# Optimization experiments

Hardware: AMD Instinct MI355X
Metric: run time of the kernel (lower is better)

Reference implementation:

```python
import jax, jax.numpy as jnp
import numpy as np

NUM_RULES = 256
IN_F = 2048
OUT_F = 2048
RANK = 8
BLOCK = 64
NUM_BLOCKS = min(IN_F, OUT_F) // BLOCK  # 32
SHARED_RANK = int(round(np.sqrt(min(IN_F, OUT_F))))  # 45
N = 16384


def setup_inputs() -> dict:
    key = jax.random.key(0)
    ks = jax.random.split(key, 7)
    x = jax.random.normal(ks[0], (N, IN_F), dtype=jnp.float32)
    rule_ids = jax.random.randint(ks[1], (N,), 0, NUM_RULES, dtype=jnp.int32)
    shared_in = jax.random.normal(ks[2], (IN_F, SHARED_RANK), dtype=jnp.float32) * (1.0 / np.sqrt(IN_F))
    shared_out = jax.random.normal(ks[3], (SHARED_RANK, OUT_F), dtype=jnp.float32) * (1.0 / np.sqrt(SHARED_RANK))
    rule_in = jax.random.normal(ks[4], (NUM_RULES, BLOCK, RANK), dtype=jnp.float32) * (1.0 / np.sqrt(BLOCK))
    rule_out = jax.random.normal(ks[5], (NUM_RULES, RANK, BLOCK), dtype=jnp.float32) * (1.0 / np.sqrt(RANK))
    rule_block_logits = jax.random.normal(ks[6], (NUM_RULES, NUM_BLOCKS), dtype=jnp.float32) * (1.0 / np.sqrt(NUM_BLOCKS))
    return {"x": x, "rule_ids": rule_ids, "shared_in": shared_in, "shared_out": shared_out,
            "rule_in": rule_in, "rule_out": rule_out, "rule_block_logits": rule_block_logits}


def reference(x, rule_ids, shared_in, shared_out, rule_in, rule_out, rule_block_logits):
    # Shared low-rank path: [N, in] @ [in, r] @ [r, out]
    base_out = (x @ shared_in) @ shared_out  # [N, OUT_F]

    total = NUM_BLOCKS * BLOCK
    x_blocks = x[:, :total].reshape(-1, NUM_BLOCKS, BLOCK)  # [N, B, bs]

    # Per-token gather of rule adapter params. This is mathematically
    # identical to the torch sort/pad/bmm/scatter path (zero padding
    # contributes zero), expressed as a dense gather + batched einsum.
    r_in = rule_in[rule_ids]    # [N, bs, RANK]
    r_out = rule_out[rule_ids]  # [N, RANK, bs]
    hidden = jnp.einsum('nbs,nsr->nbr', x_blocks, r_in)     # [N, B, RANK]
    adapter = jnp.einsum('nbr,nrs->nbs', hidden, r_out)     # [N, B, bs]

    # Block selector softmax with temperature 1/sqrt(num_blocks)
    inv_temp = jnp.sqrt(jnp.float32(NUM_BLOCKS))
    sel = jax.nn.softmax(rule_block_logits[rule_ids] * inv_temp, axis=-1)  # [N, B]
    weighted = (adapter * sel[:, :, None]).reshape(-1, total)  # [N, total]

    adapter_full = jnp.zeros_like(base_out).at[:, :total].set(weighted.astype(base_out.dtype))
    return base_out + adapter_full
```

## Files before the change

### kernel.cpp

```cpp
#include <hip/hip_runtime.h>
#include <hip/hip_bf16.h>
#include <math.h>

#define NTOK  16384
#define INF   2048
#define OUTF  2048
#define SR    45
#define RANK  8
#define BLK   64
#define NBLK  32
#define NRULE 256
#define NHIST 32
#define MAXSLOT (NTOK + NRULE * 15)
#define NTILE16 (MAXSLOT / 16)

typedef __attribute__((ext_vector_type(8))) short bf16x8;
typedef __attribute__((ext_vector_type(4))) float f32x4;
typedef __attribute__((ext_vector_type(4))) short s16x4;

typedef const __attribute__((address_space(1))) unsigned int GU32;
typedef __attribute__((address_space(3))) unsigned int LU32;

#define MFMA __builtin_amdgcn_mfma_f32_16x16x32_bf16
#define SBAR() __builtin_amdgcn_sched_barrier(0)

__device__ inline short f2bs(float f) {
    __hip_bfloat16 h = __float2bfloat16(f);
    return *reinterpret_cast<short*>(&h);
}
__device__ inline bf16x8 cvt8(const float4& a, const float4& b) {
    bf16x8 r;
    r[0] = f2bs(a.x); r[1] = f2bs(a.y); r[2] = f2bs(a.z); r[3] = f2bs(a.w);
    r[4] = f2bs(b.x); r[5] = f2bs(b.y); r[6] = f2bs(b.z); r[7] = f2bs(b.w);
    return r;
}

__global__ void kprep_a(const int* __restrict__ rule_ids,
                        const float* __restrict__ shared_in,
                        const float* __restrict__ shared_out,
                        const float* __restrict__ rule_in,
                        const float* __restrict__ rule_out,
                        unsigned short* __restrict__ ssb,
                        unsigned short* __restrict__ sob,
                        unsigned short* __restrict__ rinf,
                        unsigned short* __restrict__ rof,
                        int* __restrict__ ghist_part,
                        int* __restrict__ perm_p,
                        int* __restrict__ srid_p)
{
    if (blockIdx.x < 128) {
        const int tid = blockIdx.x * 256 + threadIdx.x;
        const int stride = 128 * 256;
        for (int idx = tid; idx < 64 * 3 * 512; idx += stride) {
            int ch = idx / 1536, rem = idx - ch * 1536;
            int nf = rem / 512;
            int l = (rem >> 3) & 63, j = idx & 7;
            int k = ch * 32 + ((l >> 4) << 3) + j;
            int col = nf * 16 + (l & 15);
            ssb[idx] = (col < SR) ? (unsigned short)f2bs(shared_in[(size_t)k * SR + col]) : 0;
        }
        for (int idx = tid; idx < 128 * 2 * 512; idx += stride) {
            int CF = idx >> 10;
            int kc = (idx >> 9) & 1;
            int l = (idx >> 3) & 63, j = idx & 7;
            int k = kc * 32 + ((l >> 4) << 3) + j;
            int col = CF * 16 + (l & 15);
            sob[idx] = (k < SR) ? (unsigned short)f2bs(shared_out[(size_t)k * OUTF + col]) : 0;
        }
        for (int idx = tid; idx < NRULE * 2 * 512; idx += stride) {
            int rid = idx >> 10;
            int half = (idx >> 9) & 1;
            int l = (idx >> 3) & 63, j = idx & 7;
            int r = l & 15;
            int s = half * 32 + ((l >> 4) << 3) + j;
            rinf[idx] = (r < RANK) ? (unsigned short)f2bs(rule_in[(size_t)rid * 512 + s * RANK + r]) : 0;
        }
        for (int idx = tid; idx < NRULE * 4 * 512; idx += stride) {
            int rid = idx >> 11;
            int cf = (idx >> 9) & 3;
            int l = (idx >> 3) & 63, j = idx & 7;
            int k = ((l >> 4) << 3) + j;
            int c = cf * 16 + (l & 15);
            rof[idx] = (k < RANK) ? (unsigned short)f2bs(rule_out[(size_t)rid * 512 + k * BLK + c]) : 0;
        }
    } else {
        __shared__ int lh[NRULE];
        const int tid = threadIdx.x;
        const int hb = blockIdx.x - 128;
        lh[tid] = 0;
        __syncthreads();
        const int base = hb * 512;
        atomicAdd(&lh[rule_ids[base + tid]], 1);
        atomicAdd(&lh[rule_ids[base + 256 + tid]], 1);
        __syncthreads();
        ghist_part[hb * NRULE + tid] = lh[tid];
        for (int j = tid; j < MAXSLOT / 32; j += 256) {
            int idx = hb * (MAXSLOT / 32) + j;
            perm_p[idx] = -1;
            srid_p[idx] = 0;
        }
    }
}

__global__ void kprep_scan(const int* __restrict__ ghist_part,
                           const float* __restrict__ logits,
                           int* __restrict__ gcnt,
                           int* __restrict__ srid_p,
                           float* __restrict__ sel_t,
                           int* __restrict__ ntot)
{
    __shared__ int sc[NRULE];
    const int tid = threadIdx.x;
    int h = 0;
#pragma unroll
    for (int b = 0; b < NHIST; ++b) h += ghist_part[b * NRULE + tid];
    const int pd = (h + 15) & ~15;
    sc[tid] = pd;
    for (int off = 1; off < NRULE; off <<= 1) {
        __syncthreads();
        int v = (tid >= off) ? sc[tid - off] : 0;
        __syncthreads();
        sc[tid] += v;
    }
    __syncthreads();
    const int excl = sc[tid] - pd;
    gcnt[tid] = excl;
    for (int q = h; q < pd; ++q) srid_p[excl + q] = tid;
    if (tid == NRULE - 1) *ntot = sc[tid];
    const float invT = 5.65685424949238f;
    const float* __restrict__ lg = logits + (size_t)tid * NBLK;
    float m = -1e30f;
    for (int b = 0; b < NBLK; ++b) m = fmaxf(m, lg[b] * invT);
    float s = 0.0f;
    for (int b = 0; b < NBLK; ++b) s += expf(lg[b] * invT - m);
    const float inv = 1.0f / s;
    for (int b = 0; b < NBLK; ++b)
        sel_t[(size_t)tid * NBLK + b] = expf(lg[b] * invT - m) * inv;
}

__global__ void kprep_scatter(const int* __restrict__ rule_ids,
                              int* __restrict__ gcnt,
                              int* __restrict__ perm_p,
                              int* __restrict__ srid_p)
{
    const int i = blockIdx.x * 256 + threadIdx.x;
    const int r = rule_ids[i];
    const int p = atomicAdd(&gcnt[r], 1);
    perm_p[p] = i;
    srid_p[p] = r;
}

__global__ __launch_bounds__(128, 4)
void kmain(const float* __restrict__ x,
           const int* __restrict__ perm_p,
           const int* __restrict__ srid_p,
           const unsigned short* __restrict__ ssb,
           const unsigned short* __restrict__ sob,
           const unsigned short* __restrict__ rinf,
           const unsigned short* __restrict__ rof,
           const float* __restrict__ sel_t,
           const int* __restrict__ ntot,
           float* __restrict__ out)
{
    __shared__ __align__(16) float xbuf[2][1024];
    __shared__ __align__(16) float hstmp[2][2][16][8];
    __shared__ __align__(16) unsigned short hs_lds[16][264];
    __shared__ __align__(16) unsigned short t_bf[16][72];

#define TRD(W, SL, C) (((float*)xbuf)[((W) * 16 + (SL)) * 52 + (C)])

    const int slot0 = blockIdx.x * 16;
    if (slot0 >= *ntot) return;

    const int tid  = threadIdx.x;
    const int lane = tid & 63;
    const int kh   = tid >> 6;
    const int row_l = lane & 15, grp = lane >> 4;

    const int rid_u = __builtin_amdgcn_readfirstlane(srid_p[slot0]);

    const int r0 = tid >> 4;
    const int u  = tid & 15;
    int tokA = perm_p[slot0 + r0];      if (tokA < 0) tokA = 0;
    int tokB = perm_p[slot0 + r0 + 8];  if (tokB < 0) tokB = 0;
    const char* gA = (const char*)(x + (size_t)tokA * INF) + ((u ^ (r0 & 7)) << 4);
    const char* gB = (const char*)(x + (size_t)tokB * INF) + ((u ^ (r0 & 7)) << 4);

#define STAGE(CH) do { \
        char* _lb = (char*)xbuf + (((CH) & 1) << 12) + (kh << 10); \
        const size_t _o = (size_t)(CH) << 8; \
        __builtin_amdgcn_global_load_lds((GU32*)(gA + _o), (LU32*)_lb,          16, 0, 0); \
        __builtin_amdgcn_global_load_lds((GU32*)(gB + _o), (LU32*)(_lb + 2048), 16, 0, 0); \
    } while (0)

    const int offA = (row_l * 16 + ((kh * 8 + grp * 2 + 0) ^ (row_l & 7))) << 4;
    const int offB = (row_l * 16 + ((kh * 8 + grp * 2 + 1) ^ (row_l & 7))) << 4;

    const bf16x8 ri = *(const bf16x8*)(rinf + ((size_t)rid_u * 2 + kh) * 512 + lane * 8);

    f32x4 aT0 = {0.f, 0.f, 0.f, 0.f};
    f32x4 aT1 = {0.f, 0.f, 0.f, 0.f};
    f32x4 aT2 = {0.f, 0.f, 0.f, 0.f};

    STAGE(0);
    __syncthreads();

    for (int ch = 0; ch < 32; ++ch) {
        if (ch < 31) STAGE(ch + 1);
        if (ch > 0) {
            const int b = ch - 1, pb = b & 1;
            const int sl = tid >> 3, r = tid & 7;
            const float v = hstmp[pb][0][sl][r] + hstmp[pb][1][sl][r];
            hs_lds[sl][b * 8 + r] =
                (unsigned short)f2bs(v * sel_t[(size_t)rid_u * NBLK + b]);
        }
        {
            const char* xb = (const char*)xbuf + ((ch & 1) << 12);
            const float4 fa = *(const float4*)(xb + offA);
            const float4 fb = *(const float4*)(xb + offB);
            const bf16x8 af = cvt8(fa, fb);
            const unsigned short* sp = ssb + (size_t)(ch * 2 + kh) * 1536 + lane * 8;
            f32x4 aH = {0.f, 0.f, 0.f, 0.f};
            aT0 = MFMA(af, *(const bf16x8*)(sp),        aT0, 0, 0, 0);
            aT1 = MFMA(af, *(const bf16x8*)(sp + 512),  aT1, 0, 0, 0);
            aT2 = MFMA(af, *(const bf16x8*)(sp + 1024), aT2, 0, 0, 0);
            aH  = MFMA(af, ri, aH, 0, 0, 0);
            if (row_l < RANK) {
#pragma unroll
                for (int q = 0; q < 4; ++q)
                    hstmp[ch & 1][kh][(grp << 2) + q][row_l] = aH[q];
            }
        }
        __syncthreads();
    }

    {
        const int b = 31, pb = 1;
        const int sl = tid >> 3, r = tid & 7;
        const float v = hstmp[pb][0][sl][r] + hstmp[pb][1][sl][r];
        hs_lds[sl][b * 8 + r] =
            (unsigned short)f2bs(v * sel_t[(size_t)rid_u * NBLK + b]);
    }
#pragma unroll
    for (int q = 0; q < 4; ++q) {
        const int sl = (grp << 2) + q;
        TRD(kh, sl, row_l)      = aT0[q];
        TRD(kh, sl, 16 + row_l) = aT1[q];
        TRD(kh, sl, 32 + row_l) = aT2[q];
    }
    __syncthreads();
    {
        const int sl = tid >> 3;
        const int cidx = tid & 7;
        if (cidx < 6) {
            const int c0 = cidx << 3;
            s16x4 v0, v1;
#pragma unroll
            for (int j = 0; j < 4; ++j) {
                v0[j] = f2bs(TRD(0, sl, c0 + j)     + TRD(1, sl, c0 + j));
                v1[j] = f2bs(TRD(0, sl, c0 + 4 + j) + TRD(1, sl, c0 + 4 + j));
            }
            *(s16x4*)(&t_bf[sl][c0])     = v0;
            *(s16x4*)(&t_bf[sl][c0 + 4]) = v1;
        } else {
            const int c0 = 48 + ((cidx - 6) << 3);
            const s16x4 z = {0, 0, 0, 0};
            *(s16x4*)(&t_bf[sl][c0])     = z;
            *(s16x4*)(&t_bf[sl][c0 + 4]) = z;
        }
    }
    __syncthreads();

    {
        const int p = kh;
        const bf16x8 at0 = *(const bf16x8*)(&t_bf[row_l][grp << 3]);
        const bf16x8 at1 = *(const bf16x8*)(&t_bf[row_l][32 + (grp << 3)]);

        bf16x8 rfv[4];
#pragma unroll
        for (int i = 0; i < 4; ++i)
            rfv[i] = *(const bf16x8*)(rof + ((size_t)rid_u * 4 + i) * 512 + lane * 8);

        const int4 pv = *(const int4*)(perm_p + slot0 + (grp << 2));
        float* const orow0 = out + (size_t)(pv.x < 0 ? 0 : pv.x) * OUTF;
        float* const orow1 = out + (size_t)(pv.y < 0 ? 0 : pv.y) * OUTF;
        float* const orow2 = out + (size_t)(pv.z < 0 ? 0 : pv.z) * OUTF;
        float* const orow3 = out + (size_t)(pv.w < 0 ? 0 : pv.w) * OUTF;

        const int CF0 = p * 64;
        const int bb0 = p * 16;
        const unsigned short* __restrict__ sobw = sob + (size_t)CF0 * 1024 + lane * 8;

        bf16x8 sb[4][2];
        bf16x8 ah[2];
        const bf16x8 zz = {0, 0, 0, 0, 0, 0, 0, 0};

#define LOADQ(SL, QI) do { \
        const unsigned short* _sp = sobw + (size_t)(QI) * 1024; \
        sb[SL][0] = *(const bf16x8*)(_sp); \
        sb[SL][1] = *(const bf16x8*)(_sp + 512); \
    } while (0)
#define LOADA(SL, BI) do { \
        ah[SL] = zz; \
        if (lane < 16) \
            ah[SL] = *(const bf16x8*)(&hs_lds[lane][(bb0 + (BI)) * 8]); \
    } while (0)

        LOADQ(0, 0); LOADQ(1, 1); LOADQ(2, 2);
        LOADA(0, 0);
        SBAR();

#pragma unroll
        for (int qi = 0; qi < 64; ++qi) {
            if (qi < 61) LOADQ((qi + 3) & 3, qi + 3);
            if ((qi & 3) == 0 && qi < 60) LOADA(((qi >> 2) + 1) & 1, (qi >> 2) + 1);
            SBAR();
            f32x4 acc = {0.f, 0.f, 0.f, 0.f};
            acc = MFMA(at0, sb[qi & 3][0], acc, 0, 0, 0);
            acc = MFMA(at1, sb[qi & 3][1], acc, 0, 0, 0);
            acc = MFMA(ah[(qi >> 2) & 1], rfv[qi & 3], acc, 0, 0, 0);
            const int col = ((CF0 + qi) << 4) + row_l;
            if (pv.x >= 0) orow0[col] = acc[0];
            if (pv.y >= 0) orow1[col] = acc[1];
            if (pv.z >= 0) orow2[col] = acc[2];
            if (pv.w >= 0) orow3[col] = acc[3];
            SBAR();
        }
#undef LOADQ
#undef LOADA
    }
}

extern "C" void kernel_launch(void* const* d_in, const int* in_sizes, int n_in,
                              void* d_out, int out_size, void* d_ws, size_t ws_size,
                              hipStream_t stream)
{
    const float* x          = (const float*)d_in[0];
    const int*   rule_ids   = (const int*)  d_in[1];
    const float* shared_in  = (const float*)d_in[2];
    const float* shared_out = (const float*)d_in[3];
    const float* rule_in    = (const float*)d_in[4];
    const float* rule_out   = (const float*)d_in[5];
    const float* logits     = (const float*)d_in[6];
    float* out = (float*)d_out;

    char* p = (char*)d_ws;
    auto carve = [&p](size_t bytes) {
        char* r = p;
        p += (bytes + 255) & ~(size_t)255;
        return r;
    };
    int*            perm_p = (int*)carve(MAXSLOT * 4);
    int*            srid_p = (int*)carve(MAXSLOT * 4);
    unsigned short* ssb    = (unsigned short*)carve(64 * 3 * 512 * 2);
    unsigned short* sob    = (unsigned short*)carve(128 * 2 * 512 * 2);
    unsigned short* rinf   = (unsigned short*)carve((size_t)NRULE * 2 * 512 * 2);
    unsigned short* rof    = (unsigned short*)carve((size_t)NRULE * 4 * 512 * 2);
    float*          sel_t  = (float*)carve((size_t)NRULE * NBLK * 4);
    int*            ghistp = (int*)carve((size_t)NHIST * NRULE * 4);
    int*            gcnt   = (int*)carve(NRULE * 4);
    int*            ntot   = (int*)carve(4);

    kprep_a<<<dim3(160), dim3(256), 0, stream>>>(
        rule_ids, shared_in, shared_out, rule_in, rule_out,
        ssb, sob, rinf, rof, ghistp, perm_p, srid_p);
    kprep_scan<<<dim3(1), dim3(256), 0, stream>>>(
        ghistp, logits, gcnt, srid_p, sel_t, ntot);
    kprep_scatter<<<dim3(64), dim3(256), 0, stream>>>(
        rule_ids, gcnt, perm_p, srid_p);
    kmain<<<dim3(NTILE16), dim3(128), 0, stream>>>(
        x, perm_p, srid_p, ssb, sob, rinf, rof, sel_t, ntot, out);
}
```

Before: 88.80 us.

## Triple-buffer x staging and register-prefetch shared weights with explicit vmcnt waits

Staging of x chunks into LDS moves from double to triple buffering with a prefetch distance of two. The shared-weight fragments become register-prefetched two chunks ahead through inline global_load_dwordx4, tracked with manual s_waitcnt vmcnt counts in place of a plain __syncthreads per iteration. The per-rule selector weights are cached in LDS once instead of being reread from global memory every chunk. The goal is to hide global-load latency in the main K loop, at the cost of more LDS and VGPRs and fragile hand-counted waitcnt logic.

```diff
diff --git a/kernel.cpp b/kernel.cpp
--- a/kernel.cpp
+++ b/kernel.cpp
@@ -23,6 +23,15 @@
 
 #define MFMA __builtin_amdgcn_mfma_f32_16x16x32_bf16
 #define SBAR() __builtin_amdgcn_sched_barrier(0)
+
+#define VMCNT(n) do { asm volatile("s_waitcnt vmcnt(" #n ")" ::: "memory"); \
+                      __builtin_amdgcn_sched_barrier(0); } while (0)
+#define BARL()   do { __builtin_amdgcn_sched_barrier(0); \
+                      asm volatile("s_waitcnt lgkmcnt(0)" ::: "memory"); \
+                      __builtin_amdgcn_s_barrier(); \
+                      __builtin_amdgcn_sched_barrier(0); } while (0)
+#define GLOAD(dst, ptr) \
+    asm volatile("global_load_dwordx4 %0, %1, off" : "=v"(dst) : "v"(ptr) : "memory")
 
 __device__ inline short f2bs(float f) {
     __hip_bfloat16 h = __float2bfloat16(f);
@@ -162,10 +171,11 @@
            const int* __restrict__ ntot,
            float* __restrict__ out)
 {
-    __shared__ __align__(16) float xbuf[2][1024];
+    __shared__ __align__(16) float xbuf[3][1024];
     __shared__ __align__(16) float hstmp[2][2][16][8];
     __shared__ __align__(16) unsigned short hs_lds[16][264];
     __shared__ __align__(16) unsigned short t_bf[16][72];
+    __shared__ float sel_lds[NBLK];
 
 #define TRD(W, SL, C) (((float*)xbuf)[((W) * 16 + (SL)) * 52 + (C)])
 
@@ -187,43 +197,55 @@
     const char* gB = (const char*)(x + (size_t)tokB * INF) + ((u ^ (r0 & 7)) << 4);
 
 #define STAGE(CH) do { \
-        char* _lb = (char*)xbuf + (((CH) & 1) << 12) + (kh << 10); \
+        char* _lb = (char*)xbuf + (size_t)((CH) % 3) * 4096 + (kh << 10); \
         const size_t _o = (size_t)(CH) << 8; \
         __builtin_amdgcn_global_load_lds((GU32*)(gA + _o), (LU32*)_lb,          16, 0, 0); \
         __builtin_amdgcn_global_load_lds((GU32*)(gB + _o), (LU32*)(_lb + 2048), 16, 0, 0); \
     } while (0)
 
+#define WLOAD(SLOT, CH) do { \
+        const unsigned short* _wp = ssb + (size_t)((CH) * 2 + kh) * 1536 + lane * 8; \
+        GLOAD(wreg[SLOT][0], _wp); \
+        GLOAD(wreg[SLOT][1], _wp + 512); \
+        GLOAD(wreg[SLOT][2], _wp + 1024); \
+    } while (0)
+
     const int offA = (row_l * 16 + ((kh * 8 + grp * 2 + 0) ^ (row_l & 7))) << 4;
     const int offB = (row_l * 16 + ((kh * 8 + grp * 2 + 1) ^ (row_l & 7))) << 4;
 
     const bf16x8 ri = *(const bf16x8*)(rinf + ((size_t)rid_u * 2 + kh) * 512 + lane * 8);
+    if (tid < NBLK) sel_lds[tid] = sel_t[(size_t)rid_u * NBLK + tid];
 
     f32x4 aT0 = {0.f, 0.f, 0.f, 0.f};
     f32x4 aT1 = {0.f, 0.f, 0.f, 0.f};
     f32x4 aT2 = {0.f, 0.f, 0.f, 0.f};
-
-    STAGE(0);
-    __syncthreads();
-
+    bf16x8 wreg[2][3];
+
+    __syncthreads();
+
+    STAGE(0); WLOAD(0, 0);
+    STAGE(1); WLOAD(1, 1);
+
+#pragma unroll
     for (int ch = 0; ch < 32; ++ch) {
-        if (ch < 31) STAGE(ch + 1);
+        if (ch < 31) VMCNT(5); else VMCNT(0);
+        BARL();
+        if (ch < 30) STAGE(ch + 2);
         if (ch > 0) {
             const int b = ch - 1, pb = b & 1;
             const int sl = tid >> 3, r = tid & 7;
             const float v = hstmp[pb][0][sl][r] + hstmp[pb][1][sl][r];
-            hs_lds[sl][b * 8 + r] =
-                (unsigned short)f2bs(v * sel_t[(size_t)rid_u * NBLK + b]);
+            hs_lds[sl][b * 8 + r] = (unsigned short)f2bs(v * sel_lds[b]);
         }
         {
-            const char* xb = (const char*)xbuf + ((ch & 1) << 12);
+            const char* xb = (const char*)xbuf + (size_t)(ch % 3) * 4096;
             const float4 fa = *(const float4*)(xb + offA);
             const float4 fb = *(const float4*)(xb + offB);
             const bf16x8 af = cvt8(fa, fb);
-            const unsigned short* sp = ssb + (size_t)(ch * 2 + kh) * 1536 + lane * 8;
             f32x4 aH = {0.f, 0.f, 0.f, 0.f};
-            aT0 = MFMA(af, *(const bf16x8*)(sp),        aT0, 0, 0, 0);
-            aT1 = MFMA(af, *(const bf16x8*)(sp + 512),  aT1, 0, 0, 0);
-            aT2 = MFMA(af, *(const bf16x8*)(sp + 1024), aT2, 0, 0, 0);
+            aT0 = MFMA(af, wreg[ch & 1][0], aT0, 0, 0, 0);
+            aT1 = MFMA(af, wreg[ch & 1][1], aT1, 0, 0, 0);
+            aT2 = MFMA(af, wreg[ch & 1][2], aT2, 0, 0, 0);
             aH  = MFMA(af, ri, aH, 0, 0, 0);
             if (row_l < RANK) {
 #pragma unroll
@@ -231,15 +253,15 @@
                     hstmp[ch & 1][kh][(grp << 2) + q][row_l] = aH[q];
             }
         }
-        __syncthreads();
-    }
+        if (ch < 30) WLOAD(ch & 1, ch + 2);
+    }
+    __syncthreads();
 
     {
         const int b = 31, pb = 1;
         const int sl = tid >> 3, r = tid & 7;
         const float v = hstmp[pb][0][sl][r] + hstmp[pb][1][sl][r];
-        hs_lds[sl][b * 8 + r] =
-            (unsigned short)f2bs(v * sel_t[(size_t)rid_u * NBLK + b]);
+        hs_lds[sl][b * 8 + r] = (unsigned short)f2bs(v * sel_lds[b]);
     }
 #pragma unroll
     for (int q = 0; q < 4; ++q) {
```

Result: no change. 88.77 us (-0.0%).

## Stage whole x tile as bf16 in LDS and split K across four waves

Applied to the files above, without the earlier changes.

Replaces the double-buffered per-chunk async global-to-LDS pipeline with a single up-front load of each 16-token tile of x. It converts the tile to bf16 in registers and stores it into a 64KB swizzled LDS buffer. The block grows to four waves that split the K dimension of the shared and rule input projections, which removes the 32 per-chunk barriers and the hstmp reduction. The partial sums are then combined across four waves, and each wave writes half as many output columns. The cost is much higher LDS use per block, which limits occupancy to about two blocks per CU, and no overlap between loading x and the MFMA work.

```diff
diff --git a/kernel.cpp b/kernel.cpp
--- a/kernel.cpp
+++ b/kernel.cpp
@@ -17,9 +17,6 @@
 typedef __attribute__((ext_vector_type(8))) short bf16x8;
 typedef __attribute__((ext_vector_type(4))) float f32x4;
 typedef __attribute__((ext_vector_type(4))) short s16x4;
-
-typedef const __attribute__((address_space(1))) unsigned int GU32;
-typedef __attribute__((address_space(3))) unsigned int LU32;
 
 #define MFMA __builtin_amdgcn_mfma_f32_16x16x32_bf16
 #define SBAR() __builtin_amdgcn_sched_barrier(0)
@@ -150,7 +147,7 @@
     srid_p[p] = r;
 }
 
-__global__ __launch_bounds__(128, 4)
+__global__ __launch_bounds__(256, 2)
 void kmain(const float* __restrict__ x,
            const int* __restrict__ perm_p,
            const int* __restrict__ srid_p,
@@ -162,117 +159,101 @@
            const int* __restrict__ ntot,
            float* __restrict__ out)
 {
-    __shared__ __align__(16) float xbuf[2][1024];
-    __shared__ __align__(16) float hstmp[2][2][16][8];
+    __shared__ __align__(16) unsigned short xbf[16 * 2048];
     __shared__ __align__(16) unsigned short hs_lds[16][264];
     __shared__ __align__(16) unsigned short t_bf[16][72];
 
-#define TRD(W, SL, C) (((float*)xbuf)[((W) * 16 + (SL)) * 52 + (C)])
+#define TRD(W, SL, C) (((float*)xbf)[((W) * 16 + (SL)) * 52 + (C)])
 
     const int slot0 = blockIdx.x * 16;
     if (slot0 >= *ntot) return;
 
     const int tid  = threadIdx.x;
     const int lane = tid & 63;
-    const int kh   = tid >> 6;
+    const int w    = tid >> 6;
     const int row_l = lane & 15, grp = lane >> 4;
 
     const int rid_u = __builtin_amdgcn_readfirstlane(srid_p[slot0]);
 
-    const int r0 = tid >> 4;
-    const int u  = tid & 15;
-    int tokA = perm_p[slot0 + r0];      if (tokA < 0) tokA = 0;
-    int tokB = perm_p[slot0 + r0 + 8];  if (tokB < 0) tokB = 0;
-    const char* gA = (const char*)(x + (size_t)tokA * INF) + ((u ^ (r0 & 7)) << 4);
-    const char* gB = (const char*)(x + (size_t)tokB * INF) + ((u ^ (r0 & 7)) << 4);
-
-#define STAGE(CH) do { \
-        char* _lb = (char*)xbuf + (((CH) & 1) << 12) + (kh << 10); \
-        const size_t _o = (size_t)(CH) << 8; \
-        __builtin_amdgcn_global_load_lds((GU32*)(gA + _o), (LU32*)_lb,          16, 0, 0); \
-        __builtin_amdgcn_global_load_lds((GU32*)(gB + _o), (LU32*)(_lb + 2048), 16, 0, 0); \
-    } while (0)
-
-    const int offA = (row_l * 16 + ((kh * 8 + grp * 2 + 0) ^ (row_l & 7))) << 4;
-    const int offB = (row_l * 16 + ((kh * 8 + grp * 2 + 1) ^ (row_l & 7))) << 4;
-
-    const bf16x8 ri = *(const bf16x8*)(rinf + ((size_t)rid_u * 2 + kh) * 512 + lane * 8);
+    {
+        const int sr = tid >> 4;
+        const int su = tid & 15;
+        int stok = perm_p[slot0 + sr];  if (stok < 0) stok = 0;
+        const float* __restrict__ xrow = x + (size_t)stok * INF;
+        const int swz = sr & 7;
+        unsigned short* __restrict__ xd = xbf + sr * 2048;
+#pragma unroll
+        for (int j = 0; j < 16; ++j) {
+            const int u8 = j * 16 + su;
+            const float4 a = *(const float4*)(xrow + (u8 << 3));
+            const float4 b = *(const float4*)(xrow + (u8 << 3) + 4);
+            *(bf16x8*)(xd + ((u8 ^ swz) << 3)) = cvt8(a, b);
+        }
+    }
+
+    const bf16x8 ri0 = *(const bf16x8*)(rinf + ((size_t)rid_u * 2 + 0) * 512 + lane * 8);
+    const bf16x8 ri1 = *(const bf16x8*)(rinf + ((size_t)rid_u * 2 + 1) * 512 + lane * 8);
+
+    __syncthreads();
 
     f32x4 aT0 = {0.f, 0.f, 0.f, 0.f};
     f32x4 aT1 = {0.f, 0.f, 0.f, 0.f};
     f32x4 aT2 = {0.f, 0.f, 0.f, 0.f};
 
-    STAGE(0);
-    __syncthreads();
-
-    for (int ch = 0; ch < 32; ++ch) {
-        if (ch < 31) STAGE(ch + 1);
-        if (ch > 0) {
-            const int b = ch - 1, pb = b & 1;
-            const int sl = tid >> 3, r = tid & 7;
-            const float v = hstmp[pb][0][sl][r] + hstmp[pb][1][sl][r];
-            hs_lds[sl][b * 8 + r] =
-                (unsigned short)f2bs(v * sel_t[(size_t)rid_u * NBLK + b]);
-        }
-        {
-            const char* xb = (const char*)xbuf + ((ch & 1) << 12);
-            const float4 fa = *(const float4*)(xb + offA);
-            const float4 fb = *(const float4*)(xb + offB);
-            const bf16x8 af = cvt8(fa, fb);
-            const unsigned short* sp = ssb + (size_t)(ch * 2 + kh) * 1536 + lane * 8;
-            f32x4 aH = {0.f, 0.f, 0.f, 0.f};
+    const int xswz = row_l & 7;
+    const unsigned short* __restrict__ xrd = xbf + row_l * 2048;
+
+#pragma unroll
+    for (int ci = 0; ci < 8; ++ci) {
+        const int c = (w << 3) + ci;
+        f32x4 aH = {0.f, 0.f, 0.f, 0.f};
+#pragma unroll
+        for (int s = 0; s < 2; ++s) {
+            const int u8 = (c << 3) + (s << 2) + grp;
+            const bf16x8 af = *(const bf16x8*)(xrd + ((u8 ^ xswz) << 3));
+            const unsigned short* __restrict__ sp =
+                ssb + (size_t)(c * 2 + s) * 1536 + lane * 8;
             aT0 = MFMA(af, *(const bf16x8*)(sp),        aT0, 0, 0, 0);
             aT1 = MFMA(af, *(const bf16x8*)(sp + 512),  aT1, 0, 0, 0);
             aT2 = MFMA(af, *(const bf16x8*)(sp + 1024), aT2, 0, 0, 0);
-            aH  = MFMA(af, ri, aH, 0, 0, 0);
-            if (row_l < RANK) {
-#pragma unroll
-                for (int q = 0; q < 4; ++q)
-                    hstmp[ch & 1][kh][(grp << 2) + q][row_l] = aH[q];
-            }
-        }
-        __syncthreads();
-    }
-
-    {
-        const int b = 31, pb = 1;
-        const int sl = tid >> 3, r = tid & 7;
-        const float v = hstmp[pb][0][sl][r] + hstmp[pb][1][sl][r];
-        hs_lds[sl][b * 8 + r] =
-            (unsigned short)f2bs(v * sel_t[(size_t)rid_u * NBLK + b]);
-    }
+            aH  = MFMA(af, s ? ri1 : ri0, aH, 0, 0, 0);
+        }
+        const float sel = sel_t[(size_t)rid_u * NBLK + c];
+        if (row_l < RANK) {
+#pragma unroll
+            for (int q = 0; q < 4; ++q)
+                hs_lds[(grp << 2) + q][c * 8 + row_l] =
+                    (unsigned short)f2bs(aH[q] * sel);
+        }
+    }
+    __syncthreads();
+
 #pragma unroll
     for (int q = 0; q < 4; ++q) {
         const int sl = (grp << 2) + q;
-        TRD(kh, sl, row_l)      = aT0[q];
-        TRD(kh, sl, 16 + row_l) = aT1[q];
-        TRD(kh, sl, 32 + row_l) = aT2[q];
+        TRD(w, sl, row_l)      = aT0[q];
+        TRD(w, sl, 16 + row_l) = aT1[q];
+        TRD(w, sl, 32 + row_l) = aT2[q];
     }
     __syncthreads();
     {
-        const int sl = tid >> 3;
-        const int cidx = tid & 7;
-        if (cidx < 6) {
-            const int c0 = cidx << 3;
-            s16x4 v0, v1;
+        const int sl = tid >> 4;
+        const int c0 = (tid & 15) << 2;
+        s16x4 v = {0, 0, 0, 0};
+        if (c0 < 48) {
 #pragma unroll
             for (int j = 0; j < 4; ++j) {
-                v0[j] = f2bs(TRD(0, sl, c0 + j)     + TRD(1, sl, c0 + j));
-                v1[j] = f2bs(TRD(0, sl, c0 + 4 + j) + TRD(1, sl, c0 + 4 + j));
+                const float sm = TRD(0, sl, c0 + j) + TRD(1, sl, c0 + j)
+                               + TRD(2, sl, c0 + j) + TRD(3, sl, c0 + j);
+                v[j] = f2bs(sm);
             }
-            *(s16x4*)(&t_bf[sl][c0])     = v0;
-            *(s16x4*)(&t_bf[sl][c0 + 4]) = v1;
-        } else {
-            const int c0 = 48 + ((cidx - 6) << 3);
-            const s16x4 z = {0, 0, 0, 0};
-            *(s16x4*)(&t_bf[sl][c0])     = z;
-            *(s16x4*)(&t_bf[sl][c0 + 4]) = z;
-        }
+        }
+        *(s16x4*)(&t_bf[sl][c0]) = v;
     }
     __syncthreads();
 
     {
-        const int p = kh;
+        const int p = w;
         const bf16x8 at0 = *(const bf16x8*)(&t_bf[row_l][grp << 3]);
         const bf16x8 at1 = *(const bf16x8*)(&t_bf[row_l][32 + (grp << 3)]);
 
@@ -287,8 +268,8 @@
         float* const orow2 = out + (size_t)(pv.z < 0 ? 0 : pv.z) * OUTF;
         float* const orow3 = out + (size_t)(pv.w < 0 ? 0 : pv.w) * OUTF;
 
-        const int CF0 = p * 64;
-        const int bb0 = p * 16;
+        const int CF0 = p * 32;
+        const int bb0 = p * 8;
         const unsigned short* __restrict__ sobw = sob + (size_t)CF0 * 1024 + lane * 8;
 
         bf16x8 sb[4][2];
@@ -311,9 +292,9 @@
         SBAR();
 
 #pragma unroll
-        for (int qi = 0; qi < 64; ++qi) {
-            if (qi < 61) LOADQ((qi + 3) & 3, qi + 3);
-            if ((qi & 3) == 0 && qi < 60) LOADA(((qi >> 2) + 1) & 1, (qi >> 2) + 1);
+        for (int qi = 0; qi < 32; ++qi) {
+            if (qi < 29) LOADQ((qi + 3) & 3, qi + 3);
+            if ((qi & 3) == 0 && qi < 28) LOADA(((qi >> 2) + 1) & 1, (qi >> 2) + 1);
             SBAR();
             f32x4 acc = {0.f, 0.f, 0.f, 0.f};
             acc = MFMA(at0, sb[qi & 3][0], acc, 0, 0, 0);
@@ -368,6 +349,6 @@
         ghistp, logits, gcnt, srid_p, sel_t, ntot);
     kprep_scatter<<<dim3(64), dim3(256), 0, stream>>>(
         rule_ids, gcnt, perm_p, srid_p);
-    kmain<<<dim3(NTILE16), dim3(128), 0, stream>>>(
+    kmain<<<dim3(NTILE16), dim3(256), 0, stream>>>(
         x, perm_p, srid_p, ssb, sob, rinf, rof, sel_t, ntot, out);
 }
```

Result: slower. 100.3 us (+12.9%).

## Split K across waves with per-wave x pipeline and register-prefetched weights

Applied to the files above, without the earlier changes.

Each wave now owns half of the K chunks (16 blocks) with its own double-buffered x staging in LDS and inline-asm prefetch of the shared_in weights into registers, waiting on vmcnt instead of block-wide barriers each chunk. The per-block hidden partials no longer need cross-wave reduction through hstmp since each wave computes full 64-wide blocks, and selector weights are preloaded. The intent is to remove the 32 per-iteration __syncthreads and hide global latency, at the cost of more LDS and registers, so occupancy drops from 4 to 3 blocks per CU.

```diff
diff --git a/kernel.cpp b/kernel.cpp
--- a/kernel.cpp
+++ b/kernel.cpp
@@ -23,6 +23,11 @@
 
 #define MFMA __builtin_amdgcn_mfma_f32_16x16x32_bf16
 #define SBAR() __builtin_amdgcn_sched_barrier(0)
+
+#define VMCNT(n) do { asm volatile("s_waitcnt vmcnt(" #n ")" ::: "memory"); \
+                      __builtin_amdgcn_sched_barrier(0); } while (0)
+#define GLOAD(dst, ptr) \
+    asm volatile("global_load_dwordx4 %0, %1, off" : "=v"(dst) : "v"(ptr) : "memory")
 
 __device__ inline short f2bs(float f) {
     __hip_bfloat16 h = __float2bfloat16(f);
@@ -150,7 +155,7 @@
     srid_p[p] = r;
 }
 
-__global__ __launch_bounds__(128, 4)
+__global__ __launch_bounds__(128, 3)
 void kmain(const float* __restrict__ x,
            const int* __restrict__ perm_p,
            const int* __restrict__ srid_p,
@@ -162,91 +167,120 @@
            const int* __restrict__ ntot,
            float* __restrict__ out)
 {
-    __shared__ __align__(16) float xbuf[2][1024];
-    __shared__ __align__(16) float hstmp[2][2][16][8];
+    __shared__ __align__(16) char xq[2][8192];
     __shared__ __align__(16) unsigned short hs_lds[16][264];
     __shared__ __align__(16) unsigned short t_bf[16][72];
 
-#define TRD(W, SL, C) (((float*)xbuf)[((W) * 16 + (SL)) * 52 + (C)])
+#define TRD(W, SL, C) (((float*)xq)[((W) * 16 + (SL)) * 52 + (C)])
 
     const int slot0 = blockIdx.x * 16;
     if (slot0 >= *ntot) return;
 
     const int tid  = threadIdx.x;
     const int lane = tid & 63;
-    const int kh   = tid >> 6;
+    const int w    = tid >> 6;
     const int row_l = lane & 15, grp = lane >> 4;
+    const int cbase = w * 16;
 
     const int rid_u = __builtin_amdgcn_readfirstlane(srid_p[slot0]);
 
-    const int r0 = tid >> 4;
-    const int u  = tid & 15;
-    int tokA = perm_p[slot0 + r0];      if (tokA < 0) tokA = 0;
-    int tokB = perm_p[slot0 + r0 + 8];  if (tokB < 0) tokB = 0;
-    const char* gA = (const char*)(x + (size_t)tokA * INF) + ((u ^ (r0 & 7)) << 4);
-    const char* gB = (const char*)(x + (size_t)tokB * INF) + ((u ^ (r0 & 7)) << 4);
-
-#define STAGE(CH) do { \
-        char* _lb = (char*)xbuf + (((CH) & 1) << 12) + (kh << 10); \
-        const size_t _o = (size_t)(CH) << 8; \
-        __builtin_amdgcn_global_load_lds((GU32*)(gA + _o), (LU32*)_lb,          16, 0, 0); \
-        __builtin_amdgcn_global_load_lds((GU32*)(gB + _o), (LU32*)(_lb + 2048), 16, 0, 0); \
-    } while (0)
-
-    const int offA = (row_l * 16 + ((kh * 8 + grp * 2 + 0) ^ (row_l & 7))) << 4;
-    const int offB = (row_l * 16 + ((kh * 8 + grp * 2 + 1) ^ (row_l & 7))) << 4;
-
-    const bf16x8 ri = *(const bf16x8*)(rinf + ((size_t)rid_u * 2 + kh) * 512 + lane * 8);
+    const char* gsrc0; const char* gsrc1; const char* gsrc2; const char* gsrc3;
+    {
+        const int u = lane & 15;
+        const char* t[4];
+#pragma unroll
+        for (int v = 0; v < 4; ++v) {
+            const int row = 4 * v + (lane >> 4);
+            int tok = perm_p[slot0 + row];
+            if (tok < 0) tok = 0;
+            t[v] = (const char*)(x + (size_t)tok * INF) + ((u ^ (row & 7)) << 4);
+        }
+        gsrc0 = t[0]; gsrc1 = t[1]; gsrc2 = t[2]; gsrc3 = t[3];
+    }
+
+    const bf16x8 ri0 = *(const bf16x8*)(rinf + ((size_t)rid_u * 2 + 0) * 512 + lane * 8);
+    const bf16x8 ri1 = *(const bf16x8*)(rinf + ((size_t)rid_u * 2 + 1) * 512 + lane * 8);
+    float sel16[16];
+#pragma unroll
+    for (int ci = 0; ci < 16; ++ci)
+        sel16[ci] = sel_t[(size_t)rid_u * NBLK + cbase + ci];
+
+    const int swz = row_l & 7;
+    const int off00 = row_l * 256 + (((0 + grp * 2 + 0) ^ swz) << 4);
+    const int off01 = row_l * 256 + (((0 + grp * 2 + 1) ^ swz) << 4);
+    const int off10 = row_l * 256 + (((8 + grp * 2 + 0) ^ swz) << 4);
+    const int off11 = row_l * 256 + (((8 + grp * 2 + 1) ^ swz) << 4);
 
     f32x4 aT0 = {0.f, 0.f, 0.f, 0.f};
     f32x4 aT1 = {0.f, 0.f, 0.f, 0.f};
     f32x4 aT2 = {0.f, 0.f, 0.f, 0.f};
-
-    STAGE(0);
+    bf16x8 wreg[2][6];
+
+    char* const xw = xq[w];
+
+#define STAGE(SL, CI) do { \
+        char* _lb = xw + ((SL) << 12); \
+        const size_t _o = (size_t)(cbase + (CI)) << 8; \
+        __builtin_amdgcn_global_load_lds((GU32*)(gsrc0 + _o), (LU32*)_lb,          16, 0, 0); \
+        __builtin_amdgcn_global_load_lds((GU32*)(gsrc1 + _o), (LU32*)(_lb + 1024), 16, 0, 0); \
+        __builtin_amdgcn_global_load_lds((GU32*)(gsrc2 + _o), (LU32*)(_lb + 2048), 16, 0, 0); \
+        __builtin_amdgcn_global_load_lds((GU32*)(gsrc3 + _o), (LU32*)(_lb + 3072), 16, 0, 0); \
+    } while (0)
+
+#define WLOAD(SL, CI) do { \
+        const unsigned short* _w0 = ssb + (size_t)((cbase + (CI)) * 2) * 1536 + lane * 8; \
+        GLOAD(wreg[SL][0], _w0); \
+        GLOAD(wreg[SL][1], _w0 + 512); \
+        GLOAD(wreg[SL][2], _w0 + 1024); \
+        GLOAD(wreg[SL][3], _w0 + 1536); \
+        GLOAD(wreg[SL][4], _w0 + 2048); \
+        GLOAD(wreg[SL][5], _w0 + 2560); \
+    } while (0)
+
+    VMCNT(0);
+
+    STAGE(0, 0); WLOAD(0, 0);
+    STAGE(1, 1); WLOAD(1, 1);
+
+#pragma unroll
+    for (int ci = 0; ci < 16; ++ci) {
+        if (ci < 15) { VMCNT(10); } else { VMCNT(0); }
+        const int sl = ci & 1;
+        const char* xb = xw + (sl << 12);
+        f32x4 aH = {0.f, 0.f, 0.f, 0.f};
+        {
+            const float4 fa0 = *(const float4*)(xb + off00);
+            const float4 fa1 = *(const float4*)(xb + off01);
+            const bf16x8 af0 = cvt8(fa0, fa1);
+            aT0 = MFMA(af0, wreg[sl][0], aT0, 0, 0, 0);
+            aT1 = MFMA(af0, wreg[sl][1], aT1, 0, 0, 0);
+            aT2 = MFMA(af0, wreg[sl][2], aT2, 0, 0, 0);
+            aH  = MFMA(af0, ri0, aH, 0, 0, 0);
+            const float4 fb0 = *(const float4*)(xb + off10);
+            const float4 fb1 = *(const float4*)(xb + off11);
+            const bf16x8 af1 = cvt8(fb0, fb1);
+            aT0 = MFMA(af1, wreg[sl][3], aT0, 0, 0, 0);
+            aT1 = MFMA(af1, wreg[sl][4], aT1, 0, 0, 0);
+            aT2 = MFMA(af1, wreg[sl][5], aT2, 0, 0, 0);
+            aH  = MFMA(af1, ri1, aH, 0, 0, 0);
+        }
+        if (row_l < RANK) {
+            const int c = cbase + ci;
+#pragma unroll
+            for (int q = 0; q < 4; ++q)
+                hs_lds[(grp << 2) + q][c * 8 + row_l] =
+                    (unsigned short)f2bs(aH[q] * sel16[ci]);
+        }
+        if (ci < 14) { STAGE(sl, ci + 2); WLOAD(sl, ci + 2); }
+    }
+
     __syncthreads();
-
-    for (int ch = 0; ch < 32; ++ch) {
-        if (ch < 31) STAGE(ch + 1);
-        if (ch > 0) {
-            const int b = ch - 1, pb = b & 1;
-            const int sl = tid >> 3, r = tid & 7;
-            const float v = hstmp[pb][0][sl][r] + hstmp[pb][1][sl][r];
-            hs_lds[sl][b * 8 + r] =
-                (unsigned short)f2bs(v * sel_t[(size_t)rid_u * NBLK + b]);
-        }
-        {
-            const char* xb = (const char*)xbuf + ((ch & 1) << 12);
-            const float4 fa = *(const float4*)(xb + offA);
-            const float4 fb = *(const float4*)(xb + offB);
-            const bf16x8 af = cvt8(fa, fb);
-            const unsigned short* sp = ssb + (size_t)(ch * 2 + kh) * 1536 + lane * 8;
-            f32x4 aH = {0.f, 0.f, 0.f, 0.f};
-            aT0 = MFMA(af, *(const bf16x8*)(sp),        aT0, 0, 0, 0);
-            aT1 = MFMA(af, *(const bf16x8*)(sp + 512),  aT1, 0, 0, 0);
-            aT2 = MFMA(af, *(const bf16x8*)(sp + 1024), aT2, 0, 0, 0);
-            aH  = MFMA(af, ri, aH, 0, 0, 0);
-            if (row_l < RANK) {
-#pragma unroll
-                for (int q = 0; q < 4; ++q)
-                    hstmp[ch & 1][kh][(grp << 2) + q][row_l] = aH[q];
-            }
-        }
-        __syncthreads();
-    }
-
-    {
-        const int b = 31, pb = 1;
-        const int sl = tid >> 3, r = tid & 7;
-        const float v = hstmp[pb][0][sl][r] + hstmp[pb][1][sl][r];
-        hs_lds[sl][b * 8 + r] =
-            (unsigned short)f2bs(v * sel_t[(size_t)rid_u * NBLK + b]);
-    }
 #pragma unroll
     for (int q = 0; q < 4; ++q) {
         const int sl = (grp << 2) + q;
-        TRD(kh, sl, row_l)      = aT0[q];
-        TRD(kh, sl, 16 + row_l) = aT1[q];
-        TRD(kh, sl, 32 + row_l) = aT2[q];
+        TRD(w, sl, row_l)      = aT0[q];
+        TRD(w, sl, 16 + row_l) = aT1[q];
+        TRD(w, sl, 32 + row_l) = aT2[q];
     }
     __syncthreads();
     {
@@ -272,7 +306,7 @@
     __syncthreads();
 
     {
-        const int p = kh;
+        const int p = w;
         const bf16x8 at0 = *(const bf16x8*)(&t_bf[row_l][grp << 3]);
         const bf16x8 at1 = *(const bf16x8*)(&t_bf[row_l][32 + (grp << 3)]);
 
```

New measurement: 106.9 us. 1.2x slower.
